# Performance work log

Hardware: AMD Instinct MI355X
Metric: run time of the kernel (lower is better)

Reference implementation:

```python
import jax, jax.numpy as jnp
import numpy as np

L, D, H, DH, DI, V, S, B = 12, 768, 12, 64, 3072, 32000, 512, 2
LN_EPS = 1e-3  # keras LayerNormalization default epsilon

def _gelu(x):
    return x * 0.5 * (1.0 + jnp.tanh(np.sqrt(2.0 / np.pi).astype(np.float32) * (x + 0.044715 * x ** 3)))

def _layer_norm(x, g, b):
    mu = jnp.mean(x, axis=-1, keepdims=True)
    var = jnp.mean((x - mu) ** 2, axis=-1, keepdims=True)
    return (x - mu) * jax.lax.rsqrt(var + LN_EPS) * g + b

def _rel_shift(x, klen):
    # x: [qlen, rlen, b, n] -> shifted [qlen, klen, b, n]
    q, r, b, n = x.shape
    x = x.reshape(r, q, b, n)[1:].reshape(q, r - 1, b, n)
    return x[:, :klen]

def _pos_emb():
    # relative positions klen..-qlen+1 (attn_type='bi', mems=None -> klen=qlen=S)
    pos_seq = jnp.arange(S, -S, -1.0, dtype=jnp.float32)                      # [2S]
    inv_freq = 1.0 / (10000.0 ** (jnp.arange(0, D, 2, dtype=jnp.float32) / D))
    sinusoid = pos_seq[:, None] * inv_freq[None, :]
    pe = jnp.concatenate([jnp.sin(sinusoid), jnp.cos(sinusoid)], axis=-1)     # [2S, D]
    return jnp.broadcast_to(pe[:, None, :], (2 * S, B, D))                    # [2S, B, D]

def setup_inputs() -> dict:
    key = jax.random.key(0)
    ks = jax.random.split(key, 12)
    rn = lambda k, sh: 0.02 * jax.random.normal(k, sh, dtype=jnp.float32)
    return {
        "inp_k": jax.random.randint(ks[0], (S, B), 0, V),
        "seg_ids": jax.random.randint(ks[1], (S, B), 0, 2),
        "input_mask": jax.random.randint(ks[2], (S, B), 0, 2),
        "lookup_table": rn(ks[3], (V, D)),
        "Wq": rn(ks[4], (L, D, H, DH)),
        "Wk": rn(ks[5], (L, D, H, DH)),
        "Wv": rn(ks[6], (L, D, H, DH)),
        "Wr": rn(ks[7], (L, D, H, DH)),
        "Wo": rn(ks[8], (L, D, H, DH)),
        "r_w_bias": rn(ks[9], (L, H, DH)),
        "r_r_bias": rn(ks[10], (L, H, DH)),
        "r_s_bias": rn(ks[11], (L, H, DH)),
        "seg_embed": rn(jax.random.fold_in(key, 100), (L, 2, H, DH)),
        "ln_attn_g": jnp.ones((L, D), jnp.float32),
        "ln_attn_b": jnp.zeros((L, D), jnp.float32),
        "ln_ff_g": jnp.ones((L, D), jnp.float32),
        "ln_ff_b": jnp.zeros((L, D), jnp.float32),
        "ff_w1": rn(jax.random.fold_in(key, 101), (L, D, DI)),
        "ff_b1": jnp.zeros((L, DI), jnp.float32),
        "ff_w2": rn(jax.random.fold_in(key, 102), (L, DI, D)),
        "ff_b2": jnp.zeros((L, D), jnp.float32),
    }

def reference(inp_k, seg_ids, input_mask, lookup_table, Wq, Wk, Wv, Wr, Wo,
              r_w_bias, r_r_bias, r_s_bias, seg_embed,
              ln_attn_g, ln_attn_b, ln_ff_g, ln_ff_b,
              ff_w1, ff_b1, ff_w2, ff_b2):
    h = lookup_table[inp_k]                                                   # [S,B,D]
    r = _pos_emb()                                                            # [2S,B,D]
    # segment "same/different" one-hot matrix [q,k,b,2]
    seg_mat = jax.nn.one_hot((seg_ids[:, None, :] != seg_ids[None, :, :]).astype(jnp.int32), 2, dtype=jnp.float32)
    attn_mask = input_mask.astype(jnp.float32)[None, :, :, None]              # [1,S,B,1] broadcast over q,heads
    scale = DH ** -0.5
    for l in range(L):
        q = jnp.einsum('ibh,hnd->ibnd', h, Wq[l])
        k = jnp.einsum('ibh,hnd->ibnd', h, Wk[l])
        v = jnp.einsum('ibh,hnd->ibnd', h, Wv[l])
        kr = jnp.einsum('ibh,hnd->ibnd', r, Wr[l])                            # [2S,B,n,d]
        ac = jnp.einsum('ibnd,jbnd->ijbn', q + r_w_bias[l], k)
        bd = _rel_shift(jnp.einsum('ibnd,jbnd->ijbn', q + r_r_bias[l], kr), S)
        ef = jnp.einsum('ibnd,snd->ibns', q + r_s_bias[l], seg_embed[l])
        ef = jnp.einsum('ijbs,ibns->ijbn', seg_mat, ef)
        score = (ac + bd + ef) * scale - 1e30 * attn_mask
        prob = jax.nn.softmax(score, axis=1)                                  # softmax over key axis j
        vec = jnp.einsum('ijbn,jbnd->ibnd', prob, v)
        h = _layer_norm(jnp.einsum('ibnd,hnd->ibh', vec, Wo[l]) + h, ln_attn_g[l], ln_attn_b[l])
        ff = _gelu(jnp.einsum('ibd,df->ibf', h, ff_w1[l]) + ff_b1[l])
        ff = jnp.einsum('ibf,fd->ibd', ff, ff_w2[l]) + ff_b2[l]
        h = _layer_norm(ff + h, ln_ff_g[l], ln_ff_b[l])
    return h
```

## Files before the change

### kernel.cpp

```cpp
#include <hip/hip_runtime.h>
#include <hip/hip_bf16.h>
#include <math.h>

#define S 512
#define B 2
#define D 768
#define H 12
#define DH 64
#define DI 3072
#define NL 12
#define NTOK (S * B)

typedef __attribute__((ext_vector_type(8))) short short8v;
typedef __attribute__((ext_vector_type(4))) float f32x4;

__device__ __forceinline__ unsigned short f2b(float f) {
  union { float f; unsigned int u; } v; v.f = f;
  unsigned int r = v.u + 0x7fffu + ((v.u >> 16) & 1u);
  return (unsigned short)(r >> 16);
}
__device__ __forceinline__ float b2f(unsigned short u) {
  union { unsigned int u; float f; } v; v.u = ((unsigned int)u) << 16;
  return v.f;
}

__device__ __forceinline__ float gelu_f(float x) {
  const float c = 0.7978845608028654f;
  float t = tanhf(c * (x + 0.044715f * x * x * x));
  return x * 0.5f * (1.0f + t);
}

__device__ __forceinline__ int vkey(int r) {
  return ((((r & 7) ^ ((r >> 3) & 7)) & 7) << 3);
}

__global__ __launch_bounds__(256) void embed_kernel(const int* __restrict__ inp_k,
                                                    const float* __restrict__ lut,
                                                    float* __restrict__ h,
                                                    unsigned short* __restrict__ h_bf) {
  int t = blockIdx.x;
  int id = inp_k[t];
  for (int j = threadIdx.x; j < D; j += 256) {
    float v = lut[(size_t)id * D + j];
    h[t * D + j] = v;
    h_bf[t * D + j] = f2b(v);
  }
}

__global__ __launch_bounds__(384) void posemb_kernel(unsigned short* __restrict__ r2b) {
  int j = blockIdx.x;
  int d = threadIdx.x;
  float pos = (float)(S - j);
  float inv_freq = expf(-logf(10000.0f) * (2.0f * (float)d / (float)D));
  float x = pos * inv_freq;
  r2b[j * D + d]       = f2b(sinf(x));
  r2b[j * D + 384 + d] = f2b(cosf(x));
}

__device__ __forceinline__ void transpose_swz(const float* __restrict__ src,
                                              unsigned short* __restrict__ dst,
                                              int K, int N, int tile, int n_base) {
  int ntk = K >> 6;
  int tk = tile % ntk, tn = tile / ntk;
  int k0 = tk << 6, n0 = tn << 6;
  int tid = threadIdx.x;
  int nl = tid >> 2, kc0 = (tid & 3) << 4;
  const float* sp = src + (size_t)(k0 + kc0) * N + n0 + nl;
  float f[16];
#pragma unroll
  for (int c = 0; c < 16; ++c) f[c] = sp[(size_t)c * N];
  short8v v0, v1;
#pragma unroll
  for (int e = 0; e < 8; ++e) {
    v0[e] = (short)f2b(f[e]);
    v1[e] = (short)f2b(f[8 + e]);
  }
  int ng = n_base + n0;
  size_t tilebase = ((size_t)(ng >> 7) * ntk + tk) * 8192;
  int row = (ng & 64) + nl;
  int key = (row & 7) << 3;
  *(short8v*)&dst[tilebase + row * 64 + (kc0 ^ key)] = v0;
  *(short8v*)&dst[tilebase + row * 64 + ((kc0 + 8) ^ key)] = v1;
}

__global__ __launch_bounds__(256) void prep_all(const float* __restrict__ Wq,
                                                const float* __restrict__ Wk,
                                                const float* __restrict__ Wv,
                                                const float* __restrict__ Wr,
                                                const float* __restrict__ Wo,
                                                const float* __restrict__ W1,
                                                const float* __restrict__ W2,
                                                unsigned short* __restrict__ wqkv_t,
                                                unsigned short* __restrict__ wr_t,
                                                unsigned short* __restrict__ wo_t,
                                                unsigned short* __restrict__ w1_t,
                                                unsigned short* __restrict__ w2_t) {
  const size_t DD = (size_t)D * D;
  const size_t DDI = (size_t)D * DI;
  int tb = blockIdx.x;
  int l = tb / 1872, t2 = tb % 1872;
  int tid = threadIdx.x;
  if (t2 < 432) {
    int which = t2 / 144, tile = t2 % 144;
    const float* src = (which == 0 ? Wq : (which == 1 ? Wk : Wv)) + l * DD;
    transpose_swz(src, wqkv_t + l * 3 * DD, D, D, tile, which * D);
  } else if (t2 < 576) {
    transpose_swz(Wr + l * DD, wr_t + l * DD, D, D, t2 - 432, 0);
  } else if (t2 < 1152) {
    transpose_swz(W1 + l * DDI, w1_t + l * DDI, D, DI, t2 - 576, 0);
  } else if (t2 < 1728) {
    transpose_swz(W2 + l * DDI, w2_t + l * DDI, DI, D, t2 - 1152, 0);
  } else {
    int c = t2 - 1728;
    int tkk = c % 12, tnn = c / 12;
    int k0 = tkk << 6, n0 = tnn << 6;
    int nl = tid >> 2, kc0 = (tid & 3) << 4;
    const float* srcp = Wo + l * DD + (size_t)(n0 + nl) * D + k0 + kc0;
    float4 a0 = *(const float4*)&srcp[0];
    float4 a1 = *(const float4*)&srcp[4];
    float4 a2 = *(const float4*)&srcp[8];
    float4 a3 = *(const float4*)&srcp[12];
    short8v v0, v1;
    v0[0] = (short)f2b(a0.x); v0[1] = (short)f2b(a0.y); v0[2] = (short)f2b(a0.z); v0[3] = (short)f2b(a0.w);
    v0[4] = (short)f2b(a1.x); v0[5] = (short)f2b(a1.y); v0[6] = (short)f2b(a1.z); v0[7] = (short)f2b(a1.w);
    v1[0] = (short)f2b(a2.x); v1[1] = (short)f2b(a2.y); v1[2] = (short)f2b(a2.z); v1[3] = (short)f2b(a2.w);
    v1[4] = (short)f2b(a3.x); v1[5] = (short)f2b(a3.y); v1[6] = (short)f2b(a3.z); v1[7] = (short)f2b(a3.w);
    unsigned short* dst = wo_t + l * DD;
    size_t tilebase = ((size_t)(n0 >> 7) * 12 + tkk) * 8192;
    int row = (n0 & 64) + nl;
    int key = (row & 7) << 3;
    *(short8v*)&dst[tilebase + row * 64 + (kc0 ^ key)] = v0;
    *(short8v*)&dst[tilebase + row * 64 + ((kc0 + 8) ^ key)] = v1;
  }
}

template <int ACT, int OUTBF>
__device__ __forceinline__ void gemm_tile(const unsigned short* __restrict__ A,
                                          const unsigned short* __restrict__ Wt,
                                          const float* __restrict__ bias,
                                          float* __restrict__ Cf,
                                          unsigned short* __restrict__ Cb,
                                          int N, int K, int bm, int bn,
                                          int kbeg, int kend) {
  __shared__ __align__(16) unsigned short As[64 * 64];
  __shared__ __align__(16) unsigned short Bs[128 * 64];
  const int tid = threadIdx.x, lane = tid & 63, w = tid >> 6;
  const int l8 = lane >> 3, lm8 = lane & 7;
  const int aColByte = ((lm8 ^ l8) << 4);
  const int KT = K >> 6;
  const size_t wtn = (size_t)(bn >> 7) * KT;

  f32x4 acc[4][2];
#pragma unroll
  for (int mi = 0; mi < 4; ++mi)
#pragma unroll
    for (int ni = 0; ni < 2; ++ni)
      acc[mi][ni] = (f32x4){0.f, 0.f, 0.f, 0.f};

  for (int kt = kbeg; kt < kend; kt += 64) {
    __syncthreads();
#pragma unroll
    for (int c = 0; c < 2; ++c) {
      int row = c * 32 + w * 8 + l8;
      const char* src = (const char*)&A[(size_t)(bm + row) * K + kt] + aColByte;
      __builtin_amdgcn_global_load_lds(
          (const __attribute__((address_space(1))) void*)src,
          (__attribute__((address_space(3))) void*)((char*)As + c * 4096 + w * 1024),
          16, 0, 0);
    }
    const char* wt = (const char*)&Wt[(wtn + (kt >> 6)) * 8192];
#pragma unroll
    for (int c = 0; c < 4; ++c) {
      __builtin_amdgcn_global_load_lds(
          (const __attribute__((address_space(1))) void*)(wt + c * 4096 + w * 1024 + lane * 16),
          (__attribute__((address_space(3))) void*)((char*)Bs + c * 4096 + w * 1024),
          16, 0, 0);
    }
    __syncthreads();
#pragma unroll
    for (int ks = 0; ks < 2; ++ks) {
      const int kus = ks * 32 + (lane >> 4) * 8;
      short8v af[4], bf[2];
#pragma unroll
      for (int mi = 0; mi < 4; ++mi) {
        int row = mi * 16 + (lane & 15);
        af[mi] = *(const short8v*)&As[row * 64 + (kus ^ ((row & 7) << 3))];
      }
#pragma unroll
      for (int ni = 0; ni < 2; ++ni) {
        int row = w * 32 + ni * 16 + (lane & 15);
        bf[ni] = *(const short8v*)&Bs[row * 64 + (kus ^ ((row & 7) << 3))];
      }
#pragma unroll
      for (int mi = 0; mi < 4; ++mi)
#pragma unroll
        for (int ni = 0; ni < 2; ++ni)
          acc[mi][ni] = __builtin_amdgcn_mfma_f32_16x16x32_bf16(af[mi], bf[ni], acc[mi][ni], 0, 0, 0);
    }
  }

  int r0 = (lane >> 4) * 4, cc = lane & 15;
#pragma unroll
  for (int mi = 0; mi < 4; ++mi) {
    int row = bm + mi * 16 + r0;
#pragma unroll
    for (int ni = 0; ni < 2; ++ni) {
      int col = bn + w * 32 + ni * 16 + cc;
      float bv = bias ? bias[col] : 0.0f;
#pragma unroll
      for (int r = 0; r < 4; ++r) {
        float v = acc[mi][ni][r] + bv;
        if (ACT == 1) v = gelu_f(v);
        if (OUTBF) Cb[(size_t)(row + r) * N + col] = f2b(v);
        else       Cf[(size_t)(row + r) * N + col] = v;
      }
    }
  }
}

__global__ __launch_bounds__(256) void gemm_qkv(const unsigned short* __restrict__ h_bf,
                                                const unsigned short* __restrict__ wqkv,
                                                unsigned short* __restrict__ qkv_bf) {
  int bx = blockIdx.x;
  gemm_tile<0, 1>(h_bf, wqkv, nullptr, nullptr, qkv_bf, 2304, 768,
                  (bx / 18) * 64, (bx % 18) * 128, 0, 768);
}

__global__ __launch_bounds__(256) void gemm_kr_all(const unsigned short* __restrict__ r2_bf,
                                                   const unsigned short* __restrict__ wr_t,
                                                   unsigned short* __restrict__ kr_all) {
  int bx = blockIdx.x;
  int l = bx / 96, b2 = bx % 96;
  gemm_tile<0, 1>(r2_bf, wr_t + (size_t)l * D * D, nullptr, nullptr,
                  kr_all + (size_t)l * NTOK * D, 768, 768,
                  (b2 / 6) * 64, (b2 % 6) * 128, 0, 768);
}

template <int ACT>
__global__ __launch_bounds__(256) void gemm_bias(const unsigned short* __restrict__ A,
                                                 const unsigned short* __restrict__ W,
                                                 const float* __restrict__ bias,
                                                 unsigned short* __restrict__ C,
                                                 int N, int K, int ncb) {
  int bx = blockIdx.x;
  gemm_tile<ACT, 1>(A, W, bias, nullptr, C, N, K, (bx / ncb) * 64, (bx % ncb) * 128, 0, K);
}

__global__ __launch_bounds__(256) void gemm_splitk(const unsigned short* __restrict__ A,
                                                   const unsigned short* __restrict__ W,
                                                   float* __restrict__ part,
                                                   int N, int K, int kch) {
  int kz = blockIdx.z;
  float* Cf = part + (size_t)kz * NTOK * N;
  gemm_tile<0, 0>(A, W, nullptr, Cf, nullptr, N, K,
                  blockIdx.y * 64, blockIdx.x * 128, kz * kch, (kz + 1) * kch);
}

__global__ __launch_bounds__(256) void attn_kernel(const unsigned short* __restrict__ qkv,
                                                   const unsigned short* __restrict__ krb,
                                                   const int* __restrict__ seg_ids,
                                                   const int* __restrict__ input_mask,
                                                   const float* __restrict__ rwb,
                                                   const float* __restrict__ rrb,
                                                   const float* __restrict__ rsb,
                                                   const float* __restrict__ segemb,
                                                   unsigned short* __restrict__ vec_bf) {
  __shared__ __align__(16) char smem[51840];
  unsigned short* qw_s = (unsigned short*)(smem + 0);
  unsigned short* qr_s = (unsigned short*)(smem + 4608);
  unsigned short* k_s  = (unsigned short*)(smem + 9216);
  unsigned short* kr_s = (unsigned short*)(smem + 18432);
  unsigned short* bd_s = (unsigned short*)(smem + 32256);
  unsigned short* vt_s = (unsigned short*)(smem + 38912);
  unsigned short* pb_s = (unsigned short*)(smem + 47104);
  float* sc_s  = (float*)(smem + 9216);
  float* efs    = (float*)(smem + 51200);
  float* frow_s = (float*)(smem + 51456);
  float* rinv_s = (float*)(smem + 51584);
  int*   segrow = (int*)(smem + 51712);

  const int it = blockIdx.x * 32, b = blockIdx.y, n = blockIdx.z;
  const int tid = threadIdx.x, lane = tid & 63, w = tid >> 6;

  {
    int il = tid >> 3, d8 = (tid & 7) * 8;
    int t = (it + il) * B + b;
    short8v q0 = *(const short8v*)&qkv[(size_t)t * 2304 + n * 64 + d8];
    short8v ow0, or0;
#pragma unroll
    for (int e = 0; e < 8; ++e) {
      float f0 = b2f((unsigned short)q0[e]);
      ow0[e] = (short)f2b(f0 + rwb[n * 64 + d8 + e]);
      or0[e] = (short)f2b(f0 + rrb[n * 64 + d8 + e]);
    }
    *(short8v*)&qw_s[il * 72 + d8] = ow0;
    *(short8v*)&qr_s[il * 72 + d8] = or0;
  }
  if (tid < 64) {
    int il = tid >> 1, s = tid & 1;
    int t = (it + il) * B + b;
    float acc = 0.0f;
    for (int d = 0; d < 64; ++d)
      acc = fmaf(b2f(qkv[(size_t)t * 2304 + n * 64 + d]) + rsb[n * 64 + d],
                 segemb[(s * H + n) * 64 + d], acc);
    efs[s * 32 + il] = acc;
  }
  if (tid < 32) segrow[tid] = seg_ids[(it + tid) * B + b];

  {
#pragma unroll
    for (int c = 0; c < 2; ++c) {
      int idx = tid + c * 256;
      int row = idx >> 3, k8 = (idx & 7) * 8;
      *(short8v*)&k_s[row * 72 + k8] =
          *(const short8v*)&qkv[(size_t)(row * B + b) * 2304 + 768 + n * 64 + k8];
    }
    int u0 = 481 - it;
#pragma unroll
    for (int c = 0; c < 3; ++c) {
      int idx = tid + c * 256;
      int row = idx >> 3, k8 = (idx & 7) * 8;
      *(short8v*)&kr_s[row * 72 + k8] =
          *(const short8v*)&krb[(size_t)(u0 + row) * 768 + n * 64 + k8];
    }
  }

  f32x4 acc_v[2];
  acc_v[0] = (f32x4){0.f, 0.f, 0.f, 0.f};
  acc_v[1] = (f32x4){0.f, 0.f, 0.f, 0.f};
  float m_run = -3.0e38f;
  float rsq = 0.0f;
  const int srow = tid >> 3, sc0 = (tid & 7) * 8;

  __syncthreads();

  for (int jt = 0; jt < 512; jt += 64) {
    const int vj = tid >> 2, vd16 = (tid & 3) * 16;
    short8v vl0 = *(const short8v*)&qkv[(size_t)((jt + vj) * B + b) * 2304 + 1536 + n * 64 + vd16];
    short8v vl1 = *(const short8v*)&qkv[(size_t)((jt + vj) * B + b) * 2304 + 1536 + n * 64 + vd16 + 8];

    f32x4 jacc[3][2];
#pragma unroll
    for (int t = 0; t < 3; ++t) {
      jacc[t][0] = (f32x4){0.f, 0.f, 0.f, 0.f};
      jacc[t][1] = (f32x4){0.f, 0.f, 0.f, 0.f};
    }
#pragma unroll
    for (int ks = 0; ks < 2; ++ks) {
      int kb = ks * 32 + (lane >> 4) * 8;
      short8v aw[2], ar[2];
#pragma unroll
      for (int mi = 0; mi < 2; ++mi) {
        aw[mi] = *(const short8v*)&qw_s[(mi * 16 + (lane & 15)) * 72 + kb];
        ar[mi] = *(const short8v*)&qr_s[(mi * 16 + (lane & 15)) * 72 + kb];
      }
      {
        short8v bk = *(const short8v*)&k_s[(w * 16 + (lane & 15)) * 72 + kb];
        jacc[0][0] = __builtin_amdgcn_mfma_f32_16x16x32_bf16(aw[0], bk, jacc[0][0], 0, 0, 0);
        jacc[0][1] = __builtin_amdgcn_mfma_f32_16x16x32_bf16(aw[1], bk, jacc[0][1], 0, 0, 0);
      }
      {
        short8v br = *(const short8v*)&kr_s[(w * 16 + (lane & 15)) * 72 + kb];
        jacc[1][0] = __builtin_amdgcn_mfma_f32_16x16x32_bf16(ar[0], br, jacc[1][0], 0, 0, 0);
        jacc[1][1] = __builtin_amdgcn_mfma_f32_16x16x32_bf16(ar[1], br, jacc[1][1], 0, 0, 0);
      }
      if (w < 2) {
        short8v br = *(const short8v*)&kr_s[((w + 4) * 16 + (lane & 15)) * 72 + kb];
        jacc[2][0] = __builtin_amdgcn_mfma_f32_16x16x32_bf16(ar[0], br, jacc[2][0], 0, 0, 0);
        jacc[2][1] = __builtin_amdgcn_mfma_f32_16x16x32_bf16(ar[1], br, jacc[2][1], 0, 0, 0);
      }
    }
#pragma unroll
    for (int t = 1; t < 3; ++t) {
      int cf = w + (t - 1) * 4;
      if (t == 1 || w < 2) {
#pragma unroll
        for (int mi = 0; mi < 2; ++mi)
#pragma unroll
          for (int r = 0; r < 4; ++r)
            bd_s[(mi * 16 + (lane >> 4) * 4 + r) * 104 + cf * 16 + (lane & 15)] =
                f2b(jacc[t][mi][r]);
      }
    }
    __syncthreads();

    {
      int jl = w * 16 + (lane & 15);
      int jg = jt + jl;
      float maskterm = -1e30f * (float)input_mask[jg * B + b];
      int segj = seg_ids[jg * B + b];
#pragma unroll
      for (int mi = 0; mi < 2; ++mi)
#pragma unroll
        for (int r = 0; r < 4; ++r) {
          int il = mi * 16 + (lane >> 4) * 4 + r;
          float bd = b2f(bd_s[il * 104 + 31 - il + jl]);
          float e = efs[(segrow[il] != segj ? 1 : 0) * 32 + il];
          sc_s[il * 68 + jl] = (jacc[0][mi][r] + bd + e) * 0.125f + maskterm;
        }
    }
    __syncthreads();

    {
      float4 f0 = *(const float4*)&sc_s[srow * 68 + sc0];
      float4 f1 = *(const float4*)&sc_s[srow * 68 + sc0 + 4];
      float mx = fmaxf(fmaxf(fmaxf(f0.x, f0.y), fmaxf(f0.z, f0.w)),
                       fmaxf(fmaxf(f1.x, f1.y), fmaxf(f1.z, f1.w)));
      mx = fmaxf(mx, __shfl_xor(mx, 1, 8));
      mx = fmaxf(mx, __shfl_xor(mx, 2, 8));
      mx = fmaxf(mx, __shfl_xor(mx, 4, 8));
      float mnew = fmaxf(m_run, mx);
      float fsc = __expf(m_run - mnew);
      m_run = mnew;
      float p0 = __expf(f0.x - mnew), p1 = __expf(f0.y - mnew);
      float p2 = __expf(f0.z - mnew), p3 = __expf(f0.w - mnew);
      float p4 = __expf(f1.x - mnew), p5 = __expf(f1.y - mnew);
      float p6 = __expf(f1.z - mnew), p7 = __expf(f1.w - mnew);
      rsq = rsq * fsc + ((p0 + p1 + p2 + p3) + (p4 + p5 + p6 + p7));
      short8v o0;
      o0[0] = (short)f2b(p0); o0[1] = (short)f2b(p1); o0[2] = (short)f2b(p2); o0[3] = (short)f2b(p3);
      o0[4] = (short)f2b(p4); o0[5] = (short)f2b(p5); o0[6] = (short)f2b(p6); o0[7] = (short)f2b(p7);
      *(short8v*)&pb_s[srow * 64 + (sc0 ^ vkey(srow))] = o0;
      if ((tid & 7) == 0) frow_s[srow] = fsc;
#pragma unroll
      for (int e = 0; e < 8; ++e) {
        int d0 = vd16 + e, d1 = vd16 + 8 + e;
        vt_s[d0 * 64 + (vj ^ vkey(d0))] = (unsigned short)vl0[e];
        vt_s[d1 * 64 + (vj ^ vkey(d1))] = (unsigned short)vl1[e];
      }
    }
    __syncthreads();

#pragma unroll
    for (int mi = 0; mi < 2; ++mi) {
#pragma unroll
      for (int r = 0; r < 4; ++r)
        acc_v[mi][r] *= frow_s[mi * 16 + (lane >> 4) * 4 + r];
    }
#pragma unroll
    for (int ks = 0; ks < 2; ++ks) {
      int kb = ks * 32 + (lane >> 4) * 8;
      int vrow = w * 16 + (lane & 15);
      short8v bv = *(const short8v*)&vt_s[vrow * 64 + (kb ^ vkey(vrow))];
#pragma unroll
      for (int mi = 0; mi < 2; ++mi) {
        int prow = mi * 16 + (lane & 15);
        short8v ap = *(const short8v*)&pb_s[prow * 64 + (kb ^ vkey(prow))];
        acc_v[mi] = __builtin_amdgcn_mfma_f32_16x16x32_bf16(ap, bv, acc_v[mi], 0, 0, 0);
      }
    }
    if (jt < 448) {
      int jn = jt + 64;
#pragma unroll
      for (int c = 0; c < 2; ++c) {
        int idx = tid + c * 256;
        int row = idx >> 3, k8 = (idx & 7) * 8;
        *(short8v*)&k_s[row * 72 + k8] =
            *(const short8v*)&qkv[(size_t)((jn + row) * B + b) * 2304 + 768 + n * 64 + k8];
      }
      int u0 = 481 - it + jn;
#pragma unroll
      for (int c = 0; c < 3; ++c) {
        int idx = tid + c * 256;
        int row = idx >> 3, k8 = (idx & 7) * 8;
        *(short8v*)&kr_s[row * 72 + k8] =
            *(const short8v*)&krb[(size_t)(u0 + row) * 768 + n * 64 + k8];
      }
    }
    __syncthreads();
  }

  {
    float tot = rsq;
    tot += __shfl_xor(tot, 1, 8);
    tot += __shfl_xor(tot, 2, 8);
    tot += __shfl_xor(tot, 4, 8);
    if ((tid & 7) == 0) rinv_s[srow] = 1.0f / tot;
  }
  __syncthreads();

#pragma unroll
  for (int mi = 0; mi < 2; ++mi)
#pragma unroll
    for (int r = 0; r < 4; ++r) {
      int row = mi * 16 + (lane >> 4) * 4 + r;
      int d = w * 16 + (lane & 15);
      int t = (it + row) * B + b;
      vec_bf[(size_t)t * D + n * 64 + d] = f2b(acc_v[mi][r] * rinv_s[row]);
    }
}

template <int P, int HASBIAS>
__global__ __launch_bounds__(256) void add_ln_reduce(const float* __restrict__ part,
                                                     const float* __restrict__ bias,
                                                     float* __restrict__ h,
                                                     unsigned short* __restrict__ h_bf,
                                                     const float* __restrict__ g,
                                                     const float* __restrict__ bi) {
  int t = blockIdx.x;
  int tid = threadIdx.x;
  __shared__ float red[256];
  float vx = 0.f, vy = 0.f, vz = 0.f, vw = 0.f;
  float s = 0.0f;
  int c = tid * 4;
  if (tid < 192) {
    float4 x = {0.f, 0.f, 0.f, 0.f};
#pragma unroll
    for (int p = 0; p < P; ++p) {
      float4 pp = *(const float4*)&part[(size_t)p * NTOK * D + (size_t)t * D + c];
      x.x += pp.x; x.y += pp.y; x.z += pp.z; x.w += pp.w;
    }
    if (HASBIAS) {
      float4 bb = *(const float4*)&bias[c];
      x.x += bb.x; x.y += bb.y; x.z += bb.z; x.w += bb.w;
    }
    float4 hh = *(const float4*)&h[(size_t)t * D + c];
    vx = x.x + hh.x; vy = x.y + hh.y; vz = x.z + hh.z; vw = x.w + hh.w;
    s = vx + vy + vz + vw;
  }
  red[tid] = s;
  __syncthreads();
  for (int st = 128; st > 0; st >>= 1) {
    if (tid < st) red[tid] += red[tid + st];
    __syncthreads();
  }
  float mu = red[0] / (float)D;
  __syncthreads();
  float s2 = 0.0f;
  if (tid < 192) {
    float dx = vx - mu, dy = vy - mu, dz = vz - mu, dw = vw - mu;
    s2 = dx * dx + dy * dy + dz * dz + dw * dw;
  }
  red[tid] = s2;
  __syncthreads();
  for (int st = 128; st > 0; st >>= 1) {
    if (tid < st) red[tid] += red[tid + st];
    __syncthreads();
  }
  float var = red[0] / (float)D;
  float rstd = rsqrtf(var + 1e-3f);
  __syncthreads();
  if (tid < 192) {
    float4 gg = *(const float4*)&g[c];
    float4 bb = *(const float4*)&bi[c];
    float o0 = (vx - mu) * rstd * gg.x + bb.x;
    float o1 = (vy - mu) * rstd * gg.y + bb.y;
    float o2 = (vz - mu) * rstd * gg.z + bb.z;
    float o3 = (vw - mu) * rstd * gg.w + bb.w;
    float4 of = {o0, o1, o2, o3};
    *(float4*)&h[(size_t)t * D + c] = of;
    ushort4 ob;
    ob.x = f2b(o0); ob.y = f2b(o1); ob.z = f2b(o2); ob.w = f2b(o3);
    *(ushort4*)&h_bf[(size_t)t * D + c] = ob;
  }
}

extern "C" void kernel_launch(void* const* d_in, const int* in_sizes, int n_in,
                              void* d_out, int out_size, void* d_ws, size_t ws_size,
                              hipStream_t stream) {
  const int*   inp_k      = (const int*)d_in[0];
  const int*   seg_ids    = (const int*)d_in[1];
  const int*   input_mask = (const int*)d_in[2];
  const float* lut        = (const float*)d_in[3];
  const float* Wq         = (const float*)d_in[4];
  const float* Wk         = (const float*)d_in[5];
  const float* Wv         = (const float*)d_in[6];
  const float* Wr         = (const float*)d_in[7];
  const float* Wo         = (const float*)d_in[8];
  const float* r_w_bias   = (const float*)d_in[9];
  const float* r_r_bias   = (const float*)d_in[10];
  const float* r_s_bias   = (const float*)d_in[11];
  const float* seg_embed  = (const float*)d_in[12];
  const float* ln_attn_g  = (const float*)d_in[13];
  const float* ln_attn_b  = (const float*)d_in[14];
  const float* ln_ff_g    = (const float*)d_in[15];
  const float* ln_ff_b    = (const float*)d_in[16];
  const float* ff_w1      = (const float*)d_in[17];
  const float* ff_b1      = (const float*)d_in[18];
  const float* ff_w2      = (const float*)d_in[19];
  const float* ff_b2      = (const float*)d_in[20];

  float* h = (float*)d_out;
  char* wp = (char*)d_ws;
  auto alloc = [&](size_t bytes) -> void* {
    void* p = (void*)wp;
    wp += (bytes + 255) & ~(size_t)255;
    return p;
  };
  const size_t TOKD = (size_t)NTOK * D;
  const size_t DD = (size_t)D * D;
  const size_t DDI = (size_t)D * DI;
  unsigned short* qkv_bf = (unsigned short*)alloc((size_t)NTOK * 2304 * 2);
  unsigned short* kr_all = (unsigned short*)alloc((size_t)NL * TOKD * 2);
  unsigned short* h_bf   = (unsigned short*)alloc(TOKD * 2);
  unsigned short* r2_bf  = (unsigned short*)alloc(TOKD * 2);
  unsigned short* vec_bf = (unsigned short*)alloc(TOKD * 2);
  unsigned short* ff1_bf = (unsigned short*)alloc((size_t)NTOK * DI * 2);
  float* part = (float*)alloc((size_t)4 * TOKD * 4);
  unsigned short* wqkv_t = (unsigned short*)alloc((size_t)NL * 3 * DD * 2);
  unsigned short* wr_t   = (unsigned short*)alloc((size_t)NL * DD * 2);
  unsigned short* wo_t   = (unsigned short*)alloc((size_t)NL * DD * 2);
  unsigned short* w1_t   = (unsigned short*)alloc((size_t)NL * DDI * 2);
  unsigned short* w2_t   = (unsigned short*)alloc((size_t)NL * DDI * 2);

  prep_all<<<NL * 1872, 256, 0, stream>>>(Wq, Wk, Wv, Wr, Wo, ff_w1, ff_w2,
                                          wqkv_t, wr_t, wo_t, w1_t, w2_t);
  embed_kernel<<<NTOK, 256, 0, stream>>>(inp_k, lut, h, h_bf);
  posemb_kernel<<<2 * S, 384, 0, stream>>>(r2_bf);
  gemm_kr_all<<<NL * 96, 256, 0, stream>>>(r2_bf, wr_t, kr_all);

  for (int l = 0; l < NL; ++l) {
    gemm_qkv<<<288, 256, 0, stream>>>(h_bf, wqkv_t + (size_t)l * 3 * DD, qkv_bf);

    attn_kernel<<<dim3(16, B, H), 256, 0, stream>>>(
        qkv_bf, kr_all + (size_t)l * TOKD, seg_ids, input_mask,
        r_w_bias + (size_t)l * D, r_r_bias + (size_t)l * D,
        r_s_bias + (size_t)l * D, seg_embed + (size_t)l * 2 * H * DH,
        vec_bf);

    gemm_splitk<<<dim3(6, 16, 2), 256, 0, stream>>>(
        vec_bf, wo_t + (size_t)l * DD, part, D, D, 384);
    add_ln_reduce<2, 0><<<NTOK, 256, 0, stream>>>(
        part, nullptr, h, h_bf, ln_attn_g + (size_t)l * D, ln_attn_b + (size_t)l * D);

    gemm_bias<1><<<24 * 16, 256, 0, stream>>>(
        h_bf, w1_t + (size_t)l * DDI, ff_b1 + (size_t)l * DI, ff1_bf, DI, D, 24);

    gemm_splitk<<<dim3(6, 16, 4), 256, 0, stream>>>(
        ff1_bf, w2_t + (size_t)l * DDI, part, D, DI, 768);
    add_ln_reduce<4, 1><<<NTOK, 256, 0, stream>>>(
        part, ff_b2 + (size_t)l * D, h, h_bf, ln_ff_g + (size_t)l * D, ln_ff_b + (size_t)l * D);
  }
}
```

Measured before the change: 1.304 ms.

## Remap GEMM blocks per XCD, stage weight transposes in LDS, retune FF2 split-K

GEMM launches become 1D grids whose block indices are remapped so consecutive tiles on each of the eight XCDs share the same weight column block, aiming to improve per-XCD L2 reuse. The FF2 split-K goes from 4 to 3 chunks, launching 288 blocks and reducing partial-sum traffic in the add+LayerNorm reduction. The weight-prep transpose now reads coalesced float4 rows into padded shared memory before writing the swizzled bf16 layout, replacing strided global loads. The risks are lower parallelism in FF2 and an extra barrier in the prep kernel.

```diff
diff --git a/kernel.cpp b/kernel.cpp
--- a/kernel.cpp
+++ b/kernel.cpp
@@ -32,6 +32,12 @@
 
 __device__ __forceinline__ int vkey(int r) {
   return ((((r & 7) ^ ((r >> 3) & 7)) & 7) << 3);
+}
+
+__device__ __forceinline__ int xcd_chunk(int orig, int nwg) {
+  int q = nwg >> 3, r = nwg & 7;
+  int x = orig & 7, o = orig >> 3;
+  return (x < r ? x * (q + 1) : r * (q + 1) + (x - r) * q) + o;
 }
 
 __global__ __launch_bounds__(256) void embed_kernel(const int* __restrict__ inp_k,
@@ -59,16 +65,27 @@
 
 __device__ __forceinline__ void transpose_swz(const float* __restrict__ src,
                                               unsigned short* __restrict__ dst,
-                                              int K, int N, int tile, int n_base) {
+                                              int K, int N, int tile, int n_base,
+                                              float* __restrict__ Ls ) {
   int ntk = K >> 6;
   int tk = tile % ntk, tn = tile / ntk;
   int k0 = tk << 6, n0 = tn << 6;
   int tid = threadIdx.x;
+  int rr = tid >> 4, c4 = (tid & 15) * 4;
+#pragma unroll
+  for (int r = 0; r < 4; ++r) {
+    int k = rr + r * 16;
+    float4 a = *(const float4*)&src[(size_t)(k0 + k) * N + n0 + c4];
+    Ls[(c4 + 0) * 65 + k] = a.x;
+    Ls[(c4 + 1) * 65 + k] = a.y;
+    Ls[(c4 + 2) * 65 + k] = a.z;
+    Ls[(c4 + 3) * 65 + k] = a.w;
+  }
+  __syncthreads();
   int nl = tid >> 2, kc0 = (tid & 3) << 4;
-  const float* sp = src + (size_t)(k0 + kc0) * N + n0 + nl;
   float f[16];
 #pragma unroll
-  for (int c = 0; c < 16; ++c) f[c] = sp[(size_t)c * N];
+  for (int c = 0; c < 16; ++c) f[c] = Ls[nl * 65 + kc0 + c];
   short8v v0, v1;
 #pragma unroll
   for (int e = 0; e < 8; ++e) {
@@ -95,6 +112,7 @@
                                                 unsigned short* __restrict__ wo_t,
                                                 unsigned short* __restrict__ w1_t,
                                                 unsigned short* __restrict__ w2_t) {
+  __shared__ float Ls[64 * 65];
   const size_t DD = (size_t)D * D;
   const size_t DDI = (size_t)D * DI;
   int tb = blockIdx.x;
@@ -103,13 +121,13 @@
   if (t2 < 432) {
     int which = t2 / 144, tile = t2 % 144;
     const float* src = (which == 0 ? Wq : (which == 1 ? Wk : Wv)) + l * DD;
-    transpose_swz(src, wqkv_t + l * 3 * DD, D, D, tile, which * D);
+    transpose_swz(src, wqkv_t + l * 3 * DD, D, D, tile, which * D, Ls);
   } else if (t2 < 576) {
-    transpose_swz(Wr + l * DD, wr_t + l * DD, D, D, t2 - 432, 0);
+    transpose_swz(Wr + l * DD, wr_t + l * DD, D, D, t2 - 432, 0, Ls);
   } else if (t2 < 1152) {
-    transpose_swz(W1 + l * DDI, w1_t + l * DDI, D, DI, t2 - 576, 0);
+    transpose_swz(W1 + l * DDI, w1_t + l * DDI, D, DI, t2 - 576, 0, Ls);
   } else if (t2 < 1728) {
-    transpose_swz(W2 + l * DDI, w2_t + l * DDI, DI, D, t2 - 1152, 0);
+    transpose_swz(W2 + l * DDI, w2_t + l * DDI, DI, D, t2 - 1152, 0, Ls);
   } else {
     int c = t2 - 1728;
     int tkk = c % 12, tnn = c / 12;
@@ -221,19 +239,21 @@
 __global__ __launch_bounds__(256) void gemm_qkv(const unsigned short* __restrict__ h_bf,
                                                 const unsigned short* __restrict__ wqkv,
                                                 unsigned short* __restrict__ qkv_bf) {
-  int bx = blockIdx.x;
+  int lin = xcd_chunk(blockIdx.x, 288);
+  int rowb = lin % 16, colb = lin / 16;
   gemm_tile<0, 1>(h_bf, wqkv, nullptr, nullptr, qkv_bf, 2304, 768,
-                  (bx / 18) * 64, (bx % 18) * 128, 0, 768);
+                  rowb * 64, colb * 128, 0, 768);
 }
 
 __global__ __launch_bounds__(256) void gemm_kr_all(const unsigned short* __restrict__ r2_bf,
                                                    const unsigned short* __restrict__ wr_t,
                                                    unsigned short* __restrict__ kr_all) {
-  int bx = blockIdx.x;
-  int l = bx / 96, b2 = bx % 96;
+  int lin = xcd_chunk(blockIdx.x, 1152);
+  int l = lin / 96, b2 = lin % 96;
+  int rowb = b2 % 16, colb = b2 / 16;
   gemm_tile<0, 1>(r2_bf, wr_t + (size_t)l * D * D, nullptr, nullptr,
                   kr_all + (size_t)l * NTOK * D, 768, 768,
-                  (b2 / 6) * 64, (b2 % 6) * 128, 0, 768);
+                  rowb * 64, colb * 128, 0, 768);
 }
 
 template <int ACT>
@@ -241,19 +261,22 @@
                                                  const unsigned short* __restrict__ W,
                                                  const float* __restrict__ bias,
                                                  unsigned short* __restrict__ C,
-                                                 int N, int K, int ncb) {
-  int bx = blockIdx.x;
-  gemm_tile<ACT, 1>(A, W, bias, nullptr, C, N, K, (bx / ncb) * 64, (bx % ncb) * 128, 0, K);
+                                                 int N, int K, int G) {
+  int lin = xcd_chunk(blockIdx.x, G);
+  int rowb = lin % 16, colb = lin / 16;
+  gemm_tile<ACT, 1>(A, W, bias, nullptr, C, N, K, rowb * 64, colb * 128, 0, K);
 }
 
 __global__ __launch_bounds__(256) void gemm_splitk(const unsigned short* __restrict__ A,
                                                    const unsigned short* __restrict__ W,
                                                    float* __restrict__ part,
-                                                   int N, int K, int kch) {
-  int kz = blockIdx.z;
-  float* Cf = part + (size_t)kz * NTOK * N;
-  gemm_tile<0, 0>(A, W, nullptr, Cf, nullptr, N, K,
-                  blockIdx.y * 64, blockIdx.x * 128, kz * kch, (kz + 1) * kch);
+                                                   int K, int kch, int G) {
+  int lin = xcd_chunk(blockIdx.x, G);
+  int kz = lin / 96, rem = lin % 96;
+  int rowb = rem % 16, colb = rem / 16;
+  float* Cf = part + (size_t)kz * NTOK * D;
+  gemm_tile<0, 0>(A, W, nullptr, Cf, nullptr, D, K,
+                  rowb * 64, colb * 128, kz * kch, (kz + 1) * kch);
 }
 
 __global__ __launch_bounds__(256) void attn_kernel(const unsigned short* __restrict__ qkv,
@@ -618,17 +641,17 @@
         r_s_bias + (size_t)l * D, seg_embed + (size_t)l * 2 * H * DH,
         vec_bf);
 
-    gemm_splitk<<<dim3(6, 16, 2), 256, 0, stream>>>(
-        vec_bf, wo_t + (size_t)l * DD, part, D, D, 384);
+    gemm_splitk<<<192, 256, 0, stream>>>(
+        vec_bf, wo_t + (size_t)l * DD, part, 768, 384, 192);
     add_ln_reduce<2, 0><<<NTOK, 256, 0, stream>>>(
         part, nullptr, h, h_bf, ln_attn_g + (size_t)l * D, ln_attn_b + (size_t)l * D);
 
-    gemm_bias<1><<<24 * 16, 256, 0, stream>>>(
-        h_bf, w1_t + (size_t)l * DDI, ff_b1 + (size_t)l * DI, ff1_bf, DI, D, 24);
-
-    gemm_splitk<<<dim3(6, 16, 4), 256, 0, stream>>>(
-        ff1_bf, w2_t + (size_t)l * DDI, part, D, DI, 768);
-    add_ln_reduce<4, 1><<<NTOK, 256, 0, stream>>>(
+    gemm_bias<1><<<384, 256, 0, stream>>>(
+        h_bf, w1_t + (size_t)l * DDI, ff_b1 + (size_t)l * DI, ff1_bf, DI, 768, 384);
+
+    gemm_splitk<<<288, 256, 0, stream>>>(
+        ff1_bf, w2_t + (size_t)l * DDI, part, 3072, 1024, 288);
+    add_ln_reduce<3, 1><<<NTOK, 256, 0, stream>>>(
         part, ff_b2 + (size_t)l * D, h, h_bf, ln_ff_g + (size_t)l * D, ln_ff_b + (size_t)l * D);
   }
 }
```

Measured after the change: 1.336 ms. 2.4% more time.
